# Kernel optimization log

Measured on AMD Instinct MI355X. Metric: run time of the kernel, lower is better.

## Reference

```python
import jax, jax.numpy as jnp
import numpy as np
import math

B, S, H, NH = 8, 2048, 128, 4
DH = H // NH
SQRT_2_OVER_PI = math.sqrt(2.0 / math.pi)


def layer_norm(x, a, b, eps=1e-6):
    # Faithful to the torch module: unbiased std (ddof=1) and divide by (std + eps)
    mean = jnp.mean(x, axis=-1, keepdims=True)
    std = jnp.std(x, axis=-1, keepdims=True, ddof=1)
    return a * (x - mean) / (std + eps) + b


def setup_inputs() -> dict:
    key = jax.random.key(0)
    ks = jax.random.split(key, 10)
    inp = {
        "hidden": jax.random.normal(ks[0], (B, S, H), dtype=jnp.float32),
        "mask": jax.random.randint(ks[1], (B, S), 0, 2, dtype=jnp.int32),
        # attention params
        "attn_scale_w": jax.random.normal(ks[2], (NH, S), dtype=jnp.float32) * 0.1,
        "Wl": jax.random.normal(ks[3], (H, H), dtype=jnp.float32) * (1.0 / math.sqrt(H)),
        "bl": jnp.zeros((H,), dtype=jnp.float32),
        # FFN params
        "W1": jax.random.normal(ks[4], (H, H), dtype=jnp.float32) * (1.0 / math.sqrt(H)),
        "b1": jnp.zeros((H,), dtype=jnp.float32),
        "ffn_scale_w": jax.random.normal(ks[5], (S, 1), dtype=jnp.float32) * 0.1,
        # layer norms
        "ln1_a": jnp.ones((H,), dtype=jnp.float32),
        "ln1_b": jnp.zeros((H,), dtype=jnp.float32),
        "ln2_a": jnp.ones((H,), dtype=jnp.float32),
        "ln2_b": jnp.zeros((H,), dtype=jnp.float32),
    }
    return inp


def reference(hidden, mask, attn_scale_w, Wl, bl, W1, b1, ffn_scale_w,
              ln1_a, ln1_b, ln2_a, ln2_b):
    x = hidden  # [B, S, H]

    # --- attention sublayer (pre-norm residual) ---
    n1 = layer_norm(x, ln1_a, ln1_b)
    qkv = n1.reshape(B, S, NH, DH).transpose(0, 2, 1, 3)  # [B, NH, S, DH]
    # scores with per-head/per-query-position learned scale
    corr = jnp.einsum("bhqd,bhkd->bhqk", qkv, qkv) / math.sqrt(DH)
    corr = corr * attn_scale_w[None, :, :, None]  # scale over query positions
    # mask over key positions: [B,1,1,S], broadcast matches repeat in torch
    corr = jnp.where(mask[:, None, None, :] == 0, -1e9, corr)
    prob = jax.nn.softmax(corr, axis=-1)
    h = jnp.einsum("bhqk,bhkd->bhqd", prob, qkv)
    h = h.transpose(0, 2, 1, 3).reshape(B, S, H)
    attn_out = h @ Wl.T + bl
    x = x + attn_out

    # --- FFN sublayer (pre-norm residual) ---
    n2 = layer_norm(x, ln2_a, ln2_b)
    hf = ffn_scale_w[None] * (n2 @ W1.T + b1)  # [B, S, H] with per-position scale
    act = 0.5 * hf * (1.0 + jnp.tanh(SQRT_2_OVER_PI * (hf + 0.044715 * hf ** 3)))
    x = x + act

    return x
```

## Files before the change

kernel.cpp:

```cpp
#include <hip/hip_runtime.h>

#define BB 8
#define SS 2048
#define HH 128
#define NHH 4
#define DHH 32

typedef _Float16 f16;
typedef f16 f16x4 __attribute__((ext_vector_type(4)));
typedef f16 f16x8 __attribute__((ext_vector_type(8)));
typedef float f32x4 __attribute__((ext_vector_type(4)));

#define BIAS0 -5.7707801636f

__device__ __forceinline__ f16x8 cat(f16x4 a, f16x4 b) {
  return (f16x8){a[0], a[1], a[2], a[3], b[0], b[1], b[2], b[3]};
}

__device__ __forceinline__ f16x4 tr_read(const f16* p) {
  f16x4 d;
  asm volatile("ds_read_b64_tr_b16 %0, %1"
               : "=v"(d)
               : "v"((__attribute__((address_space(3))) const f16*)p)
               : "memory");
  return d;
}

__global__ __launch_bounds__(256) void stage1_kernel(const float* __restrict__ x,
                                                     const float* __restrict__ ga,
                                                     const float* __restrict__ gb,
                                                     const float* __restrict__ Wl,
                                                     const float* __restrict__ W1,
                                                     const int* __restrict__ mask,
                                                     f16* __restrict__ n1,
                                                     f16* __restrict__ Wlf,
                                                     f16* __restrict__ W1f,
                                                     int* __restrict__ idx,
                                                     int* __restrict__ nkcnt,
                                                     int* __restrict__ nkpad) {
  const int tid = threadIdx.x;
  if (blockIdx.x < 1024) {
    const int wave = tid >> 6, lane = tid & 63;
    const int grp = lane >> 4, lm = lane & 15;
    const int r = wave * 4 + grp;
    const size_t row = (size_t)blockIdx.x * 16 + r;

    const float* xr = x + row * HH + lm * 8;
    float4 v0 = *(const float4*)(xr);
    float4 v1 = *(const float4*)(xr + 4);
    float xv[8] = {v0.x, v0.y, v0.z, v0.w, v1.x, v1.y, v1.z, v1.w};
    float sum = 0.f, sq = 0.f;
#pragma unroll
    for (int j = 0; j < 8; ++j) { sum += xv[j]; sq += xv[j] * xv[j]; }
#pragma unroll
    for (int m = 1; m < 16; m <<= 1) {
      sum += __shfl_xor(sum, m);
      sq += __shfl_xor(sq, m);
    }
    float mean = sum * (1.0f / HH);
    float var = fmaxf((sq - (float)HH * mean * mean) * (1.0f / (HH - 1)), 0.0f);
    float inv = 1.0f / (sqrtf(var) + 1e-6f);

    float4 a0 = *(const float4*)(ga + lm * 8);
    float4 a1 = *(const float4*)(ga + lm * 8 + 4);
    float4 b0 = *(const float4*)(gb + lm * 8);
    float4 b1 = *(const float4*)(gb + lm * 8 + 4);
    float av[8] = {a0.x, a0.y, a0.z, a0.w, a1.x, a1.y, a1.z, a1.w};
    float bv[8] = {b0.x, b0.y, b0.z, b0.w, b1.x, b1.y, b1.z, b1.w};
    f16x8 w;
#pragma unroll
    for (int j = 0; j < 8; ++j) w[j] = (f16)(av[j] * (xv[j] - mean) * inv + bv[j]);
    *(f16x8*)(n1 + row * HH + lm * 8) = w;
    return;
  }
  if (blockIdx.x < 1056) {
    int g = (blockIdx.x - 1024) * 256 + tid;
    if (g < 4096) {
      float4 w = ((const float4*)Wl)[g];
      f16x4 o = {(f16)w.x, (f16)w.y, (f16)w.z, (f16)w.w};
      ((f16x4*)Wlf)[g] = o;
    } else {
      float4 w = ((const float4*)W1)[g - 4096];
      f16x4 o = {(f16)w.x, (f16)w.y, (f16)w.z, (f16)w.w};
      ((f16x4*)W1f)[g - 4096] = o;
    }
    return;
  }
  const int b = blockIdx.x - 1056;
  __shared__ int ps[256];
  int m8[8];
  int cnt = 0;
  const int* mp = mask + b * SS + tid * 8;
#pragma unroll
  for (int j = 0; j < 8; ++j) {
    m8[j] = mp[j];
    cnt += (m8[j] != 0);
  }
  ps[tid] = cnt;
  __syncthreads();
  for (int off = 1; off < 256; off <<= 1) {
    int v = (tid >= off) ? ps[tid - off] : 0;
    __syncthreads();
    ps[tid] += v;
    __syncthreads();
  }
  int pos = ps[tid] - cnt;
#pragma unroll
  for (int j = 0; j < 8; ++j) {
    if (m8[j] != 0) idx[b * SS + pos++] = tid * 8 + j;
  }
  __syncthreads();
  int nkv = ps[255];
  int npv = (nkv + 63) & ~63;
  if (npv == 0) npv = 64;
  for (int jj = nkv + tid; jj < npv; jj += 256) idx[b * SS + jj] = 0;
  if (tid == 255) { nkcnt[b] = nkv; nkpad[b] = npv; }
}

__global__ __launch_bounds__(256, 2) void attn_kernel(const f16* __restrict__ n1,
                                                      const int* __restrict__ idx,
                                                      const int* __restrict__ nkcnt,
                                                      const int* __restrict__ nkpad,
                                                      const float* __restrict__ scalew,
                                                      f16* __restrict__ hatt) {
  const int tid = threadIdx.x;
  const int qb = blockIdx.x & 15;
  const int h = (blockIdx.x >> 4) & 3;
  const int b = blockIdx.x >> 6;
  const int wave = tid >> 6, lane = tid & 63;
  const int lg = lane >> 4, lm = lane & 15;
  const int nk = nkcnt[b];
  const int ns = nkpad[b] >> 6;

  __shared__ __align__(16) f16 Kt[2][2][64][16];
  __shared__ __align__(16) int idxL[SS];

  const f16* __restrict__ nb = n1 + (size_t)b * SS * HH + h * DHH;

  const int np = ns << 6;
  for (int j = tid * 4; j < np; j += 1024)
    *(int4*)&idxL[j] = *(const int4*)(idx + b * SS + j);

  const int q0 = qb * 128 + wave * 32 + lm;
  f16x8 qf[2];
  float sc2[2];
#pragma unroll
  for (int qt = 0; qt < 2; ++qt) {
    int q = q0 + qt * 16;
    qf[qt] = *(const f16x8*)(nb + (size_t)q * HH + lg * 8);
    sc2[qt] = scalew[h * SS + q] * 0.2550680718664f;
  }

  const int sk = tid >> 2, sp = tid & 3;

  const f32x4 zero = {0.f, 0.f, 0.f, 0.f};
  f32x4 acc[2][2] = {{zero, zero}, {zero, zero}};
  f32x4 lacc[2] = {zero, zero};
  const f16x8 ones = {(f16)1, (f16)1, (f16)1, (f16)1, (f16)1, (f16)1, (f16)1, (f16)1};

  __syncthreads();
  {
    int row = idxL[sk];
    f16x8 kreg = *(const f16x8*)(nb + (size_t)row * HH + sp * 8);
    *(f16x8*)(&Kt[0][sp >> 1][sk][(sp & 1) * 8]) = kreg;
  }
  __syncthreads();

  for (int c = 0; c < ns; ++c) {
    const int buf = c & 1;
    const int k0 = c * 64;
    f16x8 kreg;
    if (c + 1 < ns) {
      int row = idxL[k0 + 64 + sk];
      kreg = *(const f16x8*)(nb + (size_t)row * HH + sp * 8);
    }
    f16x4 t0a = tr_read(&Kt[buf][0][0][0] + lane * 4);
    f16x4 t0b = tr_read(&Kt[buf][0][16][0] + lane * 4);
    f16x4 t0c = tr_read(&Kt[buf][0][32][0] + lane * 4);
    f16x4 t0d = tr_read(&Kt[buf][0][48][0] + lane * 4);
    f16x4 t1a = tr_read(&Kt[buf][1][0][0] + lane * 4);
    f16x4 t1b = tr_read(&Kt[buf][1][16][0] + lane * 4);
    f16x4 t1c = tr_read(&Kt[buf][1][32][0] + lane * 4);
    f16x4 t1d = tr_read(&Kt[buf][1][48][0] + lane * 4);

    f16x8 kf[4];
#pragma unroll
    for (int t = 0; t < 4; ++t)
      kf[t] = *(const f16x8*)(&Kt[buf][lg >> 1][t * 16 + lm][(lg & 1) * 8]);

    const bool tail = (k0 + 64 > nk);
    f16x8 pf[2][2];
#pragma unroll
    for (int qt = 0; qt < 2; ++qt) {
#pragma unroll
      for (int t = 0; t < 4; ++t) {
        f32x4 st = __builtin_amdgcn_mfma_f32_16x16x32_f16(kf[t], qf[qt], zero, 0, 0, 0);
#pragma unroll
        for (int r = 0; r < 4; ++r) {
          float pe = __builtin_amdgcn_exp2f(st[r] * sc2[qt] + BIAS0);
          if (tail) pe = (k0 + t * 16 + lg * 4 + r < nk) ? pe : 0.0f;
          pf[qt][t >> 1][(t & 1) * 4 + r] = (f16)pe;
        }
      }
    }
#pragma unroll
    for (int qt = 0; qt < 2; ++qt) {
#pragma unroll
      for (int s = 0; s < 2; ++s)
        lacc[qt] = __builtin_amdgcn_mfma_f32_16x16x32_f16(ones, pf[qt][s], lacc[qt], 0, 0, 0);
    }

    asm volatile("s_waitcnt lgkmcnt(0)" ::: "memory");
    __builtin_amdgcn_sched_barrier(0);

    f16x8 vf;
    vf = cat(t0a, t0b);
#pragma unroll
    for (int qt = 0; qt < 2; ++qt)
      acc[qt][0] = __builtin_amdgcn_mfma_f32_16x16x32_f16(vf, pf[qt][0], acc[qt][0], 0, 0, 0);
    vf = cat(t1a, t1b);
#pragma unroll
    for (int qt = 0; qt < 2; ++qt)
      acc[qt][1] = __builtin_amdgcn_mfma_f32_16x16x32_f16(vf, pf[qt][0], acc[qt][1], 0, 0, 0);
    vf = cat(t0c, t0d);
#pragma unroll
    for (int qt = 0; qt < 2; ++qt)
      acc[qt][0] = __builtin_amdgcn_mfma_f32_16x16x32_f16(vf, pf[qt][1], acc[qt][0], 0, 0, 0);
    vf = cat(t1c, t1d);
#pragma unroll
    for (int qt = 0; qt < 2; ++qt)
      acc[qt][1] = __builtin_amdgcn_mfma_f32_16x16x32_f16(vf, pf[qt][1], acc[qt][1], 0, 0, 0);

    if (c + 1 < ns)
      *(f16x8*)(&Kt[buf ^ 1][sp >> 1][sk][(sp & 1) * 8]) = kreg;
    __syncthreads();
  }

#pragma unroll
  for (int qt = 0; qt < 2; ++qt) {
    float inv = 1.0f / lacc[qt][0];
    int q = q0 + qt * 16;
    f16* op = hatt + (size_t)(b * SS + q) * HH + h * DHH;
    f16x4 o0 = {(f16)(acc[qt][0][0] * inv), (f16)(acc[qt][0][1] * inv),
                (f16)(acc[qt][0][2] * inv), (f16)(acc[qt][0][3] * inv)};
    f16x4 o1 = {(f16)(acc[qt][1][0] * inv), (f16)(acc[qt][1][1] * inv),
                (f16)(acc[qt][1][2] * inv), (f16)(acc[qt][1][3] * inv)};
    *(f16x4*)(op + lg * 4) = o0;
    *(f16x4*)(op + 16 + lg * 4) = o1;
  }
}

__global__ __launch_bounds__(256) void mlp_kernel(const f16* __restrict__ X,
                                                  const f16* __restrict__ Wlf,
                                                  const float* __restrict__ bl,
                                                  const float* __restrict__ resid,
                                                  const float* __restrict__ ln2a,
                                                  const float* __restrict__ ln2b,
                                                  const f16* __restrict__ W1f,
                                                  const float* __restrict__ b1,
                                                  const float* __restrict__ fscale,
                                                  float* __restrict__ out) {
  const int tid = threadIdx.x;
  const int wave = tid >> 6, lane = tid & 63;
  const int lg = lane >> 4, lm = lane & 15;
  const int rbase = blockIdx.x * 32;
  const int nc0 = wave * 32;

  __shared__ __align__(16) f16 n2t[32][136];
  __shared__ float red[4][32][2];

  f32x4 acc[2][2] = {};
  const f16* xr0 = X + (size_t)(rbase + lm) * HH;
  const f16* xr1 = X + (size_t)(rbase + 16 + lm) * HH;
#pragma unroll
  for (int ks = 0; ks < 4; ++ks) {
    f16x8 bf0 = *(const f16x8*)(xr0 + ks * 32 + lg * 8);
    f16x8 bf1 = *(const f16x8*)(xr1 + ks * 32 + lg * 8);
#pragma unroll
    for (int nt = 0; nt < 2; ++nt) {
      f16x8 af = *(const f16x8*)(Wlf + (size_t)(nc0 + nt * 16 + lm) * HH + ks * 32 + lg * 8);
      acc[0][nt] = __builtin_amdgcn_mfma_f32_16x16x32_f16(af, bf0, acc[0][nt], 0, 0, 0);
      acc[1][nt] = __builtin_amdgcn_mfma_f32_16x16x32_f16(af, bf1, acc[1][nt], 0, 0, 0);
    }
  }
  float sum[2] = {0.f, 0.f}, sq[2] = {0.f, 0.f};
  f32x4 o[2][2];
#pragma unroll
  for (int g = 0; g < 2; ++g) {
    int row = rbase + g * 16 + lm;
#pragma unroll
    for (int nt = 0; nt < 2; ++nt) {
      int n = nc0 + nt * 16 + lg * 4;
      float4 rv = *(const float4*)(resid + (size_t)row * HH + n);
      float4 bv = *(const float4*)(bl + n);
      f32x4 v = acc[g][nt];
      v[0] += rv.x + bv.x; v[1] += rv.y + bv.y;
      v[2] += rv.z + bv.z; v[3] += rv.w + bv.w;
      o[g][nt] = v;
      sum[g] += v[0] + v[1] + v[2] + v[3];
      sq[g] += v[0] * v[0] + v[1] * v[1] + v[2] * v[2] + v[3] * v[3];
    }
    sum[g] += __shfl_xor(sum[g], 16); sum[g] += __shfl_xor(sum[g], 32);
    sq[g] += __shfl_xor(sq[g], 16);  sq[g] += __shfl_xor(sq[g], 32);
  }
  if (lane < 16) {
#pragma unroll
    for (int g = 0; g < 2; ++g) {
      red[wave][g * 16 + lm][0] = sum[g];
      red[wave][g * 16 + lm][1] = sq[g];
    }
  }
  __syncthreads();
#pragma unroll
  for (int g = 0; g < 2; ++g) {
    int lr = g * 16 + lm;
    float ts = red[0][lr][0] + red[1][lr][0] + red[2][lr][0] + red[3][lr][0];
    float tq = red[0][lr][1] + red[1][lr][1] + red[2][lr][1] + red[3][lr][1];
    float mean = ts * (1.0f / HH);
    float var = fmaxf((tq - (float)HH * mean * mean) * (1.0f / (HH - 1)), 0.0f);
    float inv = 1.0f / (sqrtf(var) + 1e-6f);
#pragma unroll
    for (int nt = 0; nt < 2; ++nt) {
      int n = nc0 + nt * 16 + lg * 4;
      float4 av = *(const float4*)(ln2a + n);
      float4 b2 = *(const float4*)(ln2b + n);
      f16x4 w;
      w[0] = (f16)(av.x * (o[g][nt][0] - mean) * inv + b2.x);
      w[1] = (f16)(av.y * (o[g][nt][1] - mean) * inv + b2.y);
      w[2] = (f16)(av.z * (o[g][nt][2] - mean) * inv + b2.z);
      w[3] = (f16)(av.w * (o[g][nt][3] - mean) * inv + b2.w);
      *(f16x4*)(&n2t[lr][n]) = w;
    }
  }
  __syncthreads();

  f32x4 fa[2][2] = {};
#pragma unroll
  for (int ks = 0; ks < 4; ++ks) {
    f16x8 bf0 = *(const f16x8*)(&n2t[lm][ks * 32 + lg * 8]);
    f16x8 bf1 = *(const f16x8*)(&n2t[16 + lm][ks * 32 + lg * 8]);
#pragma unroll
    for (int nt = 0; nt < 2; ++nt) {
      f16x8 af = *(const f16x8*)(W1f + (size_t)(nc0 + nt * 16 + lm) * HH + ks * 32 + lg * 8);
      fa[0][nt] = __builtin_amdgcn_mfma_f32_16x16x32_f16(af, bf0, fa[0][nt], 0, 0, 0);
      fa[1][nt] = __builtin_amdgcn_mfma_f32_16x16x32_f16(af, bf1, fa[1][nt], 0, 0, 0);
    }
  }
#pragma unroll
  for (int g = 0; g < 2; ++g) {
    int row = rbase + g * 16 + lm;
    float fs = fscale[row & (SS - 1)];
#pragma unroll
    for (int nt = 0; nt < 2; ++nt) {
      int n = nc0 + nt * 16 + lg * 4;
      float4 bv = *(const float4*)(b1 + n);
      const float* bp = &bv.x;
#pragma unroll
      for (int e = 0; e < 4; ++e) {
        float hf = fs * (fa[g][nt][e] + bp[e]);
        float u = 0.7978845608028654f * hf * (1.0f + 0.044715f * hf * hf);
        float ex = __builtin_amdgcn_exp2f(u * 2.8853900817779268f);
        float t = 1.0f - 2.0f / (ex + 1.0f);
        o[g][nt][e] += 0.5f * hf * (1.0f + t);
      }
      *(f32x4*)(out + (size_t)row * HH + n) = o[g][nt];
    }
  }
}

extern "C" void kernel_launch(void* const* d_in, const int* in_sizes, int n_in,
                              void* d_out, int out_size, void* d_ws, size_t ws_size,
                              hipStream_t stream) {
  const float* hidden = (const float*)d_in[0];
  const int* mask = (const int*)d_in[1];
  const float* scalew = (const float*)d_in[2];
  const float* Wl = (const float*)d_in[3];
  const float* bl = (const float*)d_in[4];
  const float* W1 = (const float*)d_in[5];
  const float* b1 = (const float*)d_in[6];
  const float* fscale = (const float*)d_in[7];
  const float* ln1a = (const float*)d_in[8];
  const float* ln1b = (const float*)d_in[9];
  const float* ln2a = (const float*)d_in[10];
  const float* ln2b = (const float*)d_in[11];
  float* out = (float*)d_out;

  const size_t NE = (size_t)BB * SS * HH;
  f16* n1 = (f16*)d_ws;
  f16* hattf = n1 + NE;
  f16* Wlf = hattf + NE;
  f16* W1f = Wlf + HH * HH;
  int* idx = (int*)(W1f + HH * HH);
  int* nkcnt = idx + BB * SS;
  int* nkpad = nkcnt + BB;

  stage1_kernel<<<1064, 256, 0, stream>>>(hidden, ln1a, ln1b, Wl, W1, mask,
                                          n1, Wlf, W1f, idx, nkcnt, nkpad);
  attn_kernel<<<BB * NHH * (SS / 128), 256, 0, stream>>>(n1, idx, nkcnt, nkpad,
                                                         scalew, hattf);
  mlp_kernel<<<BB * SS / 32, 256, 0, stream>>>(hattf, Wlf, bl, hidden, ln2a, ln2b,
                                               W1f, b1, fscale, out);
}
```

Measured before the change: 45.92 us.

## Give each wave a private K tile to drop block barriers in attention

Each wave now loads and double-buffers its own copy of the gathered K chunk in LDS, so the per-chunk __syncthreads disappears and waves run independently. The softmax scale is folded into Q in fp16, the constant exponent bias is dropped, and the masked tail exp loop is split into its own branch. The cost is four times the gather loads per block plus four times the K-tile LDS. Removing the bias and rounding the scaled Q to fp16 raise the risk of fp16 overflow or precision loss in the probabilities.

```diff
diff --git a/kernel.cpp b/kernel.cpp
--- a/kernel.cpp
+++ b/kernel.cpp
@@ -10,8 +10,6 @@
 typedef f16 f16x4 __attribute__((ext_vector_type(4)));
 typedef f16 f16x8 __attribute__((ext_vector_type(8)));
 typedef float f32x4 __attribute__((ext_vector_type(4)));
-
-#define BIAS0 -5.7707801636f
 
 __device__ __forceinline__ f16x8 cat(f16x4 a, f16x4 b) {
   return (f16x8){a[0], a[1], a[2], a[3], b[0], b[1], b[2], b[3]};
@@ -132,26 +130,28 @@
   const int nk = nkcnt[b];
   const int ns = nkpad[b] >> 6;
 
-  __shared__ __align__(16) f16 Kt[2][2][64][16];
+  __shared__ __align__(16) f16 Kt[4][2][2][64][16];
   __shared__ __align__(16) int idxL[SS];
 
   const f16* __restrict__ nb = n1 + (size_t)b * SS * HH + h * DHH;
-
-  const int np = ns << 6;
-  for (int j = tid * 4; j < np; j += 1024)
+  f16* __restrict__ tile = &Kt[wave][0][0][0][0];
+
+  for (int j = tid * 4; j < (ns << 6); j += 1024)
     *(int4*)&idxL[j] = *(const int4*)(idx + b * SS + j);
 
   const int q0 = qb * 128 + wave * 32 + lm;
   f16x8 qf[2];
-  float sc2[2];
 #pragma unroll
   for (int qt = 0; qt < 2; ++qt) {
     int q = q0 + qt * 16;
-    qf[qt] = *(const f16x8*)(nb + (size_t)q * HH + lg * 8);
-    sc2[qt] = scalew[h * SS + q] * 0.2550680718664f;
-  }
-
-  const int sk = tid >> 2, sp = tid & 3;
+    f16x8 raw = *(const f16x8*)(nb + (size_t)q * HH + lg * 8);
+    f16 s = (f16)(scalew[h * SS + q] * 0.2550680718664f);
+#pragma unroll
+    for (int j = 0; j < 8; ++j) raw[j] *= s;
+    qf[qt] = raw;
+  }
+
+  const int sk = lane >> 2, sp = lane & 3;
 
   const f32x4 zero = {0.f, 0.f, 0.f, 0.f};
   f32x4 acc[2][2] = {{zero, zero}, {zero, zero}};
@@ -159,50 +159,57 @@
   const f16x8 ones = {(f16)1, (f16)1, (f16)1, (f16)1, (f16)1, (f16)1, (f16)1, (f16)1};
 
   __syncthreads();
-  {
-    int row = idxL[sk];
-    f16x8 kreg = *(const f16x8*)(nb + (size_t)row * HH + sp * 8);
-    *(f16x8*)(&Kt[0][sp >> 1][sk][(sp & 1) * 8]) = kreg;
-  }
-  __syncthreads();
+
+#pragma unroll
+  for (int i = 0; i < 4; ++i) {
+    int row = idxL[i * 16 + sk];
+    f16x8 v = *(const f16x8*)(nb + (size_t)row * HH + sp * 8);
+    *(f16x8*)(tile + (sp >> 1) * 1024 + (i * 16 + sk) * 16 + (sp & 1) * 8) = v;
+  }
 
   for (int c = 0; c < ns; ++c) {
-    const int buf = c & 1;
+    const int bo = (c & 1) * 2048;
     const int k0 = c * 64;
-    f16x8 kreg;
-    if (c + 1 < ns) {
-      int row = idxL[k0 + 64 + sk];
-      kreg = *(const f16x8*)(nb + (size_t)row * HH + sp * 8);
-    }
-    f16x4 t0a = tr_read(&Kt[buf][0][0][0] + lane * 4);
-    f16x4 t0b = tr_read(&Kt[buf][0][16][0] + lane * 4);
-    f16x4 t0c = tr_read(&Kt[buf][0][32][0] + lane * 4);
-    f16x4 t0d = tr_read(&Kt[buf][0][48][0] + lane * 4);
-    f16x4 t1a = tr_read(&Kt[buf][1][0][0] + lane * 4);
-    f16x4 t1b = tr_read(&Kt[buf][1][16][0] + lane * 4);
-    f16x4 t1c = tr_read(&Kt[buf][1][32][0] + lane * 4);
-    f16x4 t1d = tr_read(&Kt[buf][1][48][0] + lane * 4);
+    f16x8 kreg[4];
+    const bool more = (c + 1 < ns);
+    if (more) {
+#pragma unroll
+      for (int i = 0; i < 4; ++i) {
+        int row = idxL[k0 + 64 + i * 16 + sk];
+        kreg[i] = *(const f16x8*)(nb + (size_t)row * HH + sp * 8);
+      }
+    }
+
+    f16x4 t0a = tr_read(tile + bo + 0 + lane * 4);
+    f16x4 t0b = tr_read(tile + bo + 256 + lane * 4);
+    f16x4 t0c = tr_read(tile + bo + 512 + lane * 4);
+    f16x4 t0d = tr_read(tile + bo + 768 + lane * 4);
+    f16x4 t1a = tr_read(tile + bo + 1024 + lane * 4);
+    f16x4 t1b = tr_read(tile + bo + 1280 + lane * 4);
+    f16x4 t1c = tr_read(tile + bo + 1536 + lane * 4);
+    f16x4 t1d = tr_read(tile + bo + 1792 + lane * 4);
 
     f16x8 kf[4];
 #pragma unroll
     for (int t = 0; t < 4; ++t)
-      kf[t] = *(const f16x8*)(&Kt[buf][lg >> 1][t * 16 + lm][(lg & 1) * 8]);
+      kf[t] = *(const f16x8*)(tile + bo + (lg >> 1) * 1024 + (t * 16 + lm) * 16 + (lg & 1) * 8);
 
     const bool tail = (k0 + 64 > nk);
     f16x8 pf[2][2];
-#pragma unroll
-    for (int qt = 0; qt < 2; ++qt) {
-#pragma unroll
-      for (int t = 0; t < 4; ++t) {
-        f32x4 st = __builtin_amdgcn_mfma_f32_16x16x32_f16(kf[t], qf[qt], zero, 0, 0, 0);
-#pragma unroll
-        for (int r = 0; r < 4; ++r) {
-          float pe = __builtin_amdgcn_exp2f(st[r] * sc2[qt] + BIAS0);
-          if (tail) pe = (k0 + t * 16 + lg * 4 + r < nk) ? pe : 0.0f;
-          pf[qt][t >> 1][(t & 1) * 4 + r] = (f16)pe;
-        }
-      }
-    }
+#define PF_LOOP(MASKED)                                                                   \
+  _Pragma("unroll") for (int qt = 0; qt < 2; ++qt) {                                      \
+    _Pragma("unroll") for (int t = 0; t < 4; ++t) {                                       \
+      f32x4 st = __builtin_amdgcn_mfma_f32_16x16x32_f16(kf[t], qf[qt], zero, 0, 0, 0);    \
+      _Pragma("unroll") for (int r = 0; r < 4; ++r) {                                     \
+        float pe = __builtin_amdgcn_exp2f(st[r]);                                         \
+        if (MASKED && (k0 + t * 16 + lg * 4 + r >= nk)) pe = 0.0f;                        \
+        pf[qt][t >> 1][(t & 1) * 4 + r] = (f16)pe;                                        \
+      }                                                                                   \
+    }                                                                                     \
+  }
+    if (!tail) { PF_LOOP(false) } else { PF_LOOP(true) }
+#undef PF_LOOP
+
 #pragma unroll
     for (int qt = 0; qt < 2; ++qt) {
 #pragma unroll
@@ -231,9 +238,12 @@
     for (int qt = 0; qt < 2; ++qt)
       acc[qt][1] = __builtin_amdgcn_mfma_f32_16x16x32_f16(vf, pf[qt][1], acc[qt][1], 0, 0, 0);
 
-    if (c + 1 < ns)
-      *(f16x8*)(&Kt[buf ^ 1][sp >> 1][sk][(sp & 1) * 8]) = kreg;
-    __syncthreads();
+    if (more) {
+      const int bn = 2048 - (c & 1) * 2048;
+#pragma unroll
+      for (int i = 0; i < 4; ++i)
+        *(f16x8*)(tile + bn + (sp >> 1) * 1024 + (i * 16 + sk) * 16 + (sp & 1) * 8) = kreg[i];
+    }
   }
 
 #pragma unroll
```

Result: faster. 40.75 us (-11.3%).
